# Kernel tuning notes

Measured on AMD Instinct MI355X. Metric: run time of the kernel, lower is better.

## Reference

```python
import jax, jax.numpy as jnp
import numpy as np

N = 262144  # points
C = 256     # backbone_out_channels
K = 20      # semantic_num_classes
BN_EPS = 1e-3
EPS = 1e-8
IGNORE = -1


def setup_inputs() -> dict:
    key = jax.random.key(0)
    ks = jax.random.split(key, 12)
    feat = jax.random.normal(ks[0], (N, C), dtype=jnp.float32)
    coord = jax.random.normal(ks[1], (N, 3), dtype=jnp.float32)
    instance_centroid = jax.random.normal(ks[2], (N, 3), dtype=jnp.float32)
    segment = jax.random.randint(ks[3], (N,), 0, K, dtype=jnp.int32)
    instance = jax.random.randint(ks[4], (N,), 0, 1000, dtype=jnp.int32)
    # bias_head: Linear(C,C) -> BN1d(C) -> ReLU -> Linear(C,3)
    w1 = jax.random.normal(ks[5], (C, C), dtype=jnp.float32) * 0.02
    b1 = jnp.zeros((C,), dtype=jnp.float32)
    gamma = jnp.ones((C,), dtype=jnp.float32)
    beta = jnp.zeros((C,), dtype=jnp.float32)
    w2 = jax.random.normal(ks[6], (C, 3), dtype=jnp.float32) * 0.02
    b2 = jnp.zeros((3,), dtype=jnp.float32)
    # seg_head: Linear(C, K)
    ws = jax.random.normal(ks[7], (C, K), dtype=jnp.float32) * 0.02
    bs = jnp.zeros((K,), dtype=jnp.float32)
    return dict(feat=feat, coord=coord, instance_centroid=instance_centroid,
                segment=segment, instance=instance,
                w1=w1, b1=b1, gamma=gamma, beta=beta, w2=w2, b2=b2, ws=ws, bs=bs)


def reference(feat, coord, instance_centroid, segment, instance,
              w1, b1, gamma, beta, w2, b2, ws, bs):
    # bias head: Linear -> BatchNorm1d (training stats) -> ReLU -> Linear
    h = feat @ w1 + b1                                  # [N, C]
    mu = jnp.mean(h, axis=0)
    var = jnp.mean((h - mu) ** 2, axis=0)               # biased var (torch BN)
    h = (h - mu) * jax.lax.rsqrt(var + BN_EPS) * gamma + beta
    h = jax.nn.relu(h)
    bias_pred = h @ w2 + b2                             # [N, 3]

    logit_pred = feat @ ws + bs                         # [N, K]

    # semantic cross-entropy with ignore_index
    valid = segment != IGNORE
    tgt = jnp.where(valid, segment, 0)
    logp = jax.nn.log_softmax(logit_pred, axis=-1)
    nll = -jnp.take_along_axis(logp, tgt[:, None], axis=1)[:, 0]
    vf = valid.astype(logit_pred.dtype)
    seg_loss = jnp.sum(nll * vf) / (jnp.sum(vf) + EPS)

    # masked bias L1 loss
    mask = (instance != IGNORE).astype(bias_pred.dtype)
    bias_gt = instance_centroid - coord                 # [N, 3]
    bias_dist = jnp.sum(jnp.abs(bias_pred - bias_gt), axis=-1)
    msum = jnp.sum(mask) + EPS
    bias_l1_loss = jnp.sum(bias_dist * mask) / msum

    # masked cosine (direction) loss
    pred_n = bias_pred / (jnp.linalg.norm(bias_pred, axis=1, keepdims=True) + EPS)
    gt_n = bias_gt / (jnp.linalg.norm(bias_gt, axis=1, keepdims=True) + EPS)
    cos = -jnp.sum(pred_n * gt_n, axis=-1)
    bias_cosine_loss = jnp.sum(cos * mask) / msum

    loss = seg_loss + bias_l1_loss + bias_cosine_loss
    return jnp.stack([loss, seg_loss, bias_l1_loss, bias_cosine_loss])
```

## Files before the change

kernel.cpp:

```cpp
#include <hip/hip_runtime.h>
#include <cstdio>
#include <cstdint>

typedef unsigned int u32;
typedef unsigned short u16;
typedef short bf16x8 __attribute__((ext_vector_type(8)));
typedef float f32x4 __attribute__((ext_vector_type(4)));

#define NPTS 262144
#define CDIM 256
#define KCLS 20
#define NBLK 4096
#define NSLOT 256
#define LSLOT 64

#define OFF_WT    ((size_t)134217728)
#define OFF_AGGBN (OFF_WT + (size_t)163840)
#define OFF_AGGNL (OFF_AGGBN + (size_t)524288)
#define OFF_AGGL  (OFF_AGGNL + (size_t)2048)
#define OFF_AB    (OFF_AGGL + (size_t)1024)
#define WS_NEED   (OFF_AB + (size_t)2048)
#define MEMSET_OFF OFF_AGGBN
#define MEMSET_LEN ((size_t)(524288 + 2048 + 1024))

__device__ __forceinline__ u16 bf16rne(float x) {
    u32 u = __float_as_uint(x);
    u32 r = u + 0x7FFFu + ((u >> 16) & 1u);
    return (u16)(r >> 16);
}
__device__ __forceinline__ float bf2f(u16 b) {
    return __uint_as_float(((u32)b) << 16);
}

__global__ void k_prep(const float* __restrict__ w1, const float* __restrict__ wsm,
                       u16* __restrict__ Wt) {
    int k = blockIdx.x;
    int n = threadIdx.x;
    float v = 0.f;
    if (n < 256) v = w1[k * 256 + n];
    else if (n < 256 + KCLS) v = wsm[k * KCLS + (n - 256)];
    Wt[n * 256 + k] = bf16rne(v);
}

__global__ __launch_bounds__(256) void k_gemm(
    const float* __restrict__ feat, const float* __restrict__ b1,
    const float* __restrict__ bs, const int* __restrict__ segment,
    const u16* __restrict__ Wt, u16* __restrict__ h_out,
    float* __restrict__ aggBN, float* __restrict__ aggNLL)
{
    __shared__ uint4 smem4[2112];
    uint4* const As4 = smem4;
    uint4* const Bs4 = smem4 + 256;

    const int t = threadIdx.x;
    const int lane = t & 63;
    const int wv = t >> 6;
    const int q = lane >> 4;
    const int i16 = lane & 15;
    const int row0 = blockIdx.x * 64;
    const int slot = blockIdx.x & (NSLOT - 1);

    const f32x4 fz = {0.f, 0.f, 0.f, 0.f};
    f32x4 acc[4][4];
    f32x4 lacc[2];
#pragma unroll
    for (int r = 0; r < 4; ++r)
#pragma unroll
        for (int c = 0; c < 4; ++c) acc[r][c] = fz;
    lacc[0] = fz; lacc[1] = fz;

    const int sm = t >> 2;
    const int sq = t & 3;
    const float* fsrc = feat + (size_t)(row0 + sm) * 256 + sq * 8;
    const int As_wslot = sq * 64 + (sm ^ (sq << 2));

    float4 f0 = *(const float4*)(fsrc);
    float4 f1 = *(const float4*)(fsrc + 4);

#pragma unroll 1
    for (int kc = 0; kc < 8; ++kc) {
        const int k0 = kc * 32;
        {
            uint4 pk;
            pk.x = (u32)bf16rne(f0.x) | ((u32)bf16rne(f0.y) << 16);
            pk.y = (u32)bf16rne(f0.z) | ((u32)bf16rne(f0.w) << 16);
            pk.z = (u32)bf16rne(f1.x) | ((u32)bf16rne(f1.y) << 16);
            pk.w = (u32)bf16rne(f1.z) | ((u32)bf16rne(f1.w) << 16);
            As4[As_wslot] = pk;
        }
#pragma unroll
        for (int i = 0; i < 5; ++i) {
            const u16* src = Wt + (size_t)(i * 64 + lane) * 256 + k0 + wv * 8;
            u32* dst = (u32*)&Bs4[wv * 320 + i * 64];
            __builtin_amdgcn_global_load_lds(
                (const __attribute__((address_space(1))) u32*)src,
                (__attribute__((address_space(3))) u32*)dst, 16, 0, 0);
        }
        __syncthreads();

        float4 fn0, fn1;
        if (kc < 7) {
            fn0 = *(const float4*)(fsrc + (kc + 1) * 32);
            fn1 = *(const float4*)(fsrc + (kc + 1) * 32 + 4);
        }

        bf16x8 af[4], bfr[4], lbf[2], la;
#pragma unroll
        for (int r = 0; r < 4; ++r)
            af[r] = *(const bf16x8*)&As4[q * 64 + ((r * 16 + i16) ^ (q << 2))];
        la = *(const bf16x8*)&As4[q * 64 + ((wv * 16 + i16) ^ (q << 2))];
#pragma unroll
        for (int c = 0; c < 4; ++c)
            bfr[c] = *(const bf16x8*)&Bs4[q * 320 + wv * 64 + c * 16 + i16];
#pragma unroll
        for (int x = 0; x < 2; ++x)
            lbf[x] = *(const bf16x8*)&Bs4[q * 320 + 256 + x * 16 + i16];

#pragma unroll
        for (int r = 0; r < 4; ++r)
#pragma unroll
            for (int c = 0; c < 4; ++c)
                acc[r][c] = __builtin_amdgcn_mfma_f32_16x16x32_bf16(af[r], bfr[c], acc[r][c], 0, 0, 0);
#pragma unroll
        for (int x = 0; x < 2; ++x)
            lacc[x] = __builtin_amdgcn_mfma_f32_16x16x32_bf16(la, lbf[x], lacc[x], 0, 0, 0);
        __syncthreads();
        f0 = fn0; f1 = fn1;
    }

    float b1v[4];
#pragma unroll
    for (int c = 0; c < 4; ++c) b1v[c] = b1[wv * 64 + c * 16 + i16];
    float bsv0 = bs[i16];
    float bsv1 = (16 + i16 < KCLS) ? bs[16 + i16] : 0.f;

    float nllacc = 0.f, cntacc = 0.f;
#pragma unroll
    for (int j = 0; j < 4; ++j) {
        int rowr = row0 + wv * 16 + q * 4 + j;
        float l0 = lacc[0][j] + bsv0;
        float l1raw = lacc[1][j] + bsv1;
        float l1m = (i16 < 4) ? l1raw : -3.0e38f;
        float mx = fmaxf(l0, l1m);
#pragma unroll
        for (int d = 1; d < 16; d <<= 1) mx = fmaxf(mx, __shfl_xor(mx, d));
        float s = __expf(l0 - mx) + ((i16 < 4) ? __expf(l1raw - mx) : 0.f);
#pragma unroll
        for (int d = 1; d < 16; d <<= 1) s += __shfl_xor(s, d);
        int tg = segment[rowr];
        float v0 = __shfl(l0, (lane & 48) + (tg & 15));
        float v1 = __shfl(l1raw, (lane & 48) + ((tg - 16) & 15));
        float lt = (tg < 16) ? v0 : v1;
        if (i16 == 0 && tg >= 0) {
            nllacc += __logf(s) + mx - lt;
            cntacc += 1.f;
        }
    }
#pragma unroll
    for (int d = 1; d < 64; d <<= 1) {
        nllacc += __shfl_xor(nllacc, d);
        cntacc += __shfl_xor(cntacc, d);
    }
    if (t == 0) { atomicAdd(aggNLL + slot * 2, 0.f); }
    if (lane == 0) {
        atomicAdd(aggNLL + slot * 2 + 0, nllacc);
        atomicAdd(aggNLL + slot * 2 + 1, cntacc);
    }

#pragma unroll
    for (int c = 0; c < 4; ++c) {
        float s1 = 0.f, s2 = 0.f;
#pragma unroll
        for (int r = 0; r < 4; ++r)
#pragma unroll
            for (int j = 0; j < 4; ++j) {
                float v = acc[r][c][j] + b1v[c];
                s1 += v; s2 = fmaf(v, v, s2);
            }
        s1 += __shfl_xor(s1, 16); s1 += __shfl_xor(s1, 32);
        s2 += __shfl_xor(s2, 16); s2 += __shfl_xor(s2, 32);
        if (q == 0) {
            int ch = wv * 64 + c * 16 + i16;
            atomicAdd(aggBN + slot * 512 + ch, s1);
            atomicAdd(aggBN + slot * 512 + 256 + ch, s2);
        }
    }

    u16* Ht = (u16*)smem4;
#pragma unroll
    for (int r = 0; r < 4; ++r)
#pragma unroll
        for (int c = 0; c < 4; ++c)
#pragma unroll
            for (int j = 0; j < 4; ++j) {
                float v = acc[r][c][j] + b1v[c];
                int rw = r * 16 + q * 4 + j;
                int cl = wv * 64 + c * 16 + i16;
                Ht[rw * 264 + cl] = bf16rne(v);
            }
    __syncthreads();
#pragma unroll
    for (int i = 0; i < 8; ++i) {
        int chunk = i * 256 + t;
        int m = chunk >> 5;
        int off = (chunk & 31) * 16;
        uint4 v = *(const uint4*)((const char*)smem4 + m * 528 + off);
        *(uint4*)((char*)h_out + (size_t)(row0 + m) * 512 + off) = v;
    }
}

__global__ void k_reduce(const float* __restrict__ gamma, const float* __restrict__ beta,
                         const float* __restrict__ aggBN,
                         float* __restrict__ Aarr, float* __restrict__ Barr) {
    int c = threadIdx.x;
    float s1 = 0.f, s2 = 0.f;
    for (int s = 0; s < NSLOT; ++s) {
        s1 += aggBN[s * 512 + c];
        s2 += aggBN[s * 512 + 256 + c];
    }
    const float inv = 1.f / (float)NPTS;
    float mu = s1 * inv;
    float var = fmaxf(s2 * inv - mu * mu, 0.f);
    float a = gamma[c] * rsqrtf(var + 1e-3f);
    Aarr[c] = a;
    Barr[c] = beta[c] - mu * a;
}

__global__ __launch_bounds__(256) void k_loss(
    const u16* __restrict__ h, const float* __restrict__ Aarr, const float* __restrict__ Barr,
    const float* __restrict__ w2, const float* __restrict__ b2,
    const float* __restrict__ coord, const float* __restrict__ cent,
    const int* __restrict__ inst, float* __restrict__ aggL)
{
    __shared__ float red[12];
    const int t = threadIdx.x;
    const int lane = t & 63;
    const int wv = t >> 6;
    const int rowbase = blockIdx.x * 128 + wv * 32;
    const int c4 = lane * 4;

    float4 Av = *(const float4*)(Aarr + c4);
    float4 Bv = *(const float4*)(Barr + c4);
    float4 wa = *(const float4*)(w2 + lane * 12);
    float4 wb = *(const float4*)(w2 + lane * 12 + 4);
    float4 wc = *(const float4*)(w2 + lane * 12 + 8);
    float b2x = b2[0], b2y = b2[1], b2z = b2[2];

    float l1a = 0.f, cosa = 0.f, ma = 0.f;
    for (int rr = 0; rr < 32; ++rr) {
        int row = rowbase + rr;
        ushort4 u = *(const ushort4*)(h + (size_t)row * 256 + c4);
        float t0 = fmaxf(fmaf(bf2f(u.x), Av.x, Bv.x), 0.f);
        float t1 = fmaxf(fmaf(bf2f(u.y), Av.y, Bv.y), 0.f);
        float t2 = fmaxf(fmaf(bf2f(u.z), Av.z, Bv.z), 0.f);
        float t3 = fmaxf(fmaf(bf2f(u.w), Av.w, Bv.w), 0.f);
        float p0 = fmaf(t0, wa.x, fmaf(t1, wa.w, fmaf(t2, wb.z, t3 * wc.y)));
        float p1 = fmaf(t0, wa.y, fmaf(t1, wb.x, fmaf(t2, wb.w, t3 * wc.z)));
        float p2 = fmaf(t0, wa.z, fmaf(t1, wb.y, fmaf(t2, wc.x, t3 * wc.w)));
#pragma unroll
        for (int d = 1; d < 64; d <<= 1) {
            p0 += __shfl_xor(p0, d);
            p1 += __shfl_xor(p1, d);
            p2 += __shfl_xor(p2, d);
        }
        if (lane == 0) {
            float bpx = p0 + b2x, bpy = p1 + b2y, bpz = p2 + b2z;
            const float* cp = coord + (size_t)row * 3;
            const float* ip = cent + (size_t)row * 3;
            float gx = ip[0] - cp[0], gy = ip[1] - cp[1], gz = ip[2] - cp[2];
            float mk = (inst[row] != -1) ? 1.f : 0.f;
            float l1 = fabsf(bpx - gx) + fabsf(bpy - gy) + fabsf(bpz - gz);
            float np = sqrtf(fmaf(bpx, bpx, fmaf(bpy, bpy, bpz * bpz)));
            float ng = sqrtf(fmaf(gx, gx, fmaf(gy, gy, gz * gz)));
            float dp = fmaf(bpx, gx, fmaf(bpy, gy, bpz * gz));
            float cosv = -dp / ((np + 1e-8f) * (ng + 1e-8f));
            l1a = fmaf(l1, mk, l1a);
            cosa = fmaf(cosv, mk, cosa);
            ma += mk;
        }
    }
    if (lane == 0) { red[wv] = l1a; red[4 + wv] = cosa; red[8 + wv] = ma; }
    __syncthreads();
    if (t == 0) {
        int slot = blockIdx.x & (LSLOT - 1);
        atomicAdd(aggL + slot * 4 + 0, red[0] + red[1] + red[2] + red[3]);
        atomicAdd(aggL + slot * 4 + 1, red[4] + red[5] + red[6] + red[7]);
        atomicAdd(aggL + slot * 4 + 2, red[8] + red[9] + red[10] + red[11]);
    }
}

__global__ void k_final(const float* __restrict__ aggNLL, const float* __restrict__ aggL,
                        float* __restrict__ out) {
    int lane = threadIdx.x;
    float nll = 0.f, cnt = 0.f;
#pragma unroll
    for (int i = 0; i < 4; ++i) {
        int s = lane + i * 64;
        nll += aggNLL[s * 2 + 0];
        cnt += aggNLL[s * 2 + 1];
    }
    float l1 = aggL[lane * 4 + 0];
    float cs = aggL[lane * 4 + 1];
    float mk = aggL[lane * 4 + 2];
#pragma unroll
    for (int d = 1; d < 64; d <<= 1) {
        nll += __shfl_xor(nll, d);
        cnt += __shfl_xor(cnt, d);
        l1 += __shfl_xor(l1, d);
        cs += __shfl_xor(cs, d);
        mk += __shfl_xor(mk, d);
    }
    if (lane == 0) {
        float seg = nll / (cnt + 1e-8f);
        float l1l = l1 / (mk + 1e-8f);
        float csl = cs / (mk + 1e-8f);
        out[0] = seg + l1l + csl;
        out[1] = seg;
        out[2] = l1l;
        out[3] = csl;
    }
}

extern "C" void kernel_launch(void* const* d_in, const int* in_sizes, int n_in,
                              void* d_out, int out_size, void* d_ws, size_t ws_size,
                              hipStream_t stream) {
    const float* feat   = (const float*)d_in[0];
    const float* coord  = (const float*)d_in[1];
    const float* cent   = (const float*)d_in[2];
    const int* segment  = (const int*)d_in[3];
    const int* inst     = (const int*)d_in[4];
    const float* w1     = (const float*)d_in[5];
    const float* b1     = (const float*)d_in[6];
    const float* gamma  = (const float*)d_in[7];
    const float* beta   = (const float*)d_in[8];
    const float* w2     = (const float*)d_in[9];
    const float* b2     = (const float*)d_in[10];
    const float* wsm    = (const float*)d_in[11];
    const float* bs     = (const float*)d_in[12];
    float* out = (float*)d_out;

    char* wsb = (char*)d_ws;
    u16* h_ws    = (u16*)wsb;
    u16* Wt      = (u16*)(wsb + OFF_WT);
    float* aggBN = (float*)(wsb + OFF_AGGBN);
    float* aggNL = (float*)(wsb + OFF_AGGNL);
    float* aggL  = (float*)(wsb + OFF_AGGL);
    float* Aarr  = (float*)(wsb + OFF_AB);
    float* Barr  = Aarr + 256;

    if (ws_size < WS_NEED)
        fprintf(stderr, "kernel_launch: ws_size=%zu < needed %zu — WILL CORRUPT\n",
                ws_size, (size_t)WS_NEED);

    hipMemsetAsync(wsb + MEMSET_OFF, 0, MEMSET_LEN, stream);
    k_prep<<<256, 320, 0, stream>>>(w1, wsm, Wt);
    k_gemm<<<NBLK, 256, 0, stream>>>(feat, b1, bs, segment, Wt, h_ws, aggBN, aggNL);
    k_reduce<<<1, 256, 0, stream>>>(gamma, beta, aggBN, Aarr, Barr);
    k_loss<<<2048, 256, 0, stream>>>(h_ws, Aarr, Barr, w2, b2, coord, cent, inst, aggL);
    k_final<<<1, 64, 0, stream>>>(aggNL, aggL, out);
}
```

Measured before the change: 550.1 us.

## Double GEMM row tile, parallelize BN reduce, use MFMA for bias head projection

The main GEMM kernel now processes 128 rows per block (two A sub-tiles sharing each B tile load) with an occupancy hint of two blocks per CU, which halves B-tile traffic per row. The BN statistics reduction is spread over 256 blocks with wave shuffles instead of one block looping serially. The loss kernel replaces the per-row 64-lane shuffle reduction with a bf16 MFMA against a zero-padded w2 fragment, processing 16 rows per MFMA. This adds register pressure in the GEMM, and rounding the normalized activations to bf16 before the second linear layer changes precision slightly.

```diff
diff --git a/kernel.cpp b/kernel.cpp
--- a/kernel.cpp
+++ b/kernel.cpp
@@ -10,7 +10,7 @@
 #define NPTS 262144
 #define CDIM 256
 #define KCLS 20
-#define NBLK 4096
+#define NBLK 2048
 #define NSLOT 256
 #define LSLOT 64
 
@@ -42,7 +42,7 @@
     Wt[n * 256 + k] = bf16rne(v);
 }
 
-__global__ __launch_bounds__(256) void k_gemm(
+__global__ __launch_bounds__(256, 2) void k_gemm(
     const float* __restrict__ feat, const float* __restrict__ b1,
     const float* __restrict__ bs, const int* __restrict__ segment,
     const u16* __restrict__ Wt, u16* __restrict__ h_out,
@@ -50,32 +50,36 @@
 {
     __shared__ uint4 smem4[2112];
     uint4* const As4 = smem4;
-    uint4* const Bs4 = smem4 + 256;
+    uint4* const Bs4 = smem4 + 512;
 
     const int t = threadIdx.x;
     const int lane = t & 63;
     const int wv = t >> 6;
     const int q = lane >> 4;
     const int i16 = lane & 15;
-    const int row0 = blockIdx.x * 64;
+    const int row0 = blockIdx.x * 128;
     const int slot = blockIdx.x & (NSLOT - 1);
 
     const f32x4 fz = {0.f, 0.f, 0.f, 0.f};
-    f32x4 acc[4][4];
-    f32x4 lacc[2];
-#pragma unroll
-    for (int r = 0; r < 4; ++r)
+    f32x4 acc[8][4];
+    f32x4 lacc[2][2];
+#pragma unroll
+    for (int r = 0; r < 8; ++r)
 #pragma unroll
         for (int c = 0; c < 4; ++c) acc[r][c] = fz;
-    lacc[0] = fz; lacc[1] = fz;
+    lacc[0][0] = fz; lacc[0][1] = fz; lacc[1][0] = fz; lacc[1][1] = fz;
 
     const int sm = t >> 2;
     const int sq = t & 3;
-    const float* fsrc = feat + (size_t)(row0 + sm) * 256 + sq * 8;
-    const int As_wslot = sq * 64 + (sm ^ (sq << 2));
-
-    float4 f0 = *(const float4*)(fsrc);
-    float4 f1 = *(const float4*)(fsrc + 4);
+    const float* fsrcA = feat + (size_t)(row0 + sm) * 256 + sq * 8;
+    const float* fsrcB = feat + (size_t)(row0 + 64 + sm) * 256 + sq * 8;
+    const int As_wslotA = sq * 128 + (sm ^ (sq << 2));
+    const int As_wslotB = sq * 128 + ((sm + 64) ^ (sq << 2));
+
+    float4 f0 = *(const float4*)(fsrcA);
+    float4 f1 = *(const float4*)(fsrcA + 4);
+    float4 g0 = *(const float4*)(fsrcB);
+    float4 g1 = *(const float4*)(fsrcB + 4);
 
 #pragma unroll 1
     for (int kc = 0; kc < 8; ++kc) {
@@ -86,7 +90,12 @@
             pk.y = (u32)bf16rne(f0.z) | ((u32)bf16rne(f0.w) << 16);
             pk.z = (u32)bf16rne(f1.x) | ((u32)bf16rne(f1.y) << 16);
             pk.w = (u32)bf16rne(f1.z) | ((u32)bf16rne(f1.w) << 16);
-            As4[As_wslot] = pk;
+            As4[As_wslotA] = pk;
+            pk.x = (u32)bf16rne(g0.x) | ((u32)bf16rne(g0.y) << 16);
+            pk.y = (u32)bf16rne(g0.z) | ((u32)bf16rne(g0.w) << 16);
+            pk.z = (u32)bf16rne(g1.x) | ((u32)bf16rne(g1.y) << 16);
+            pk.w = (u32)bf16rne(g1.z) | ((u32)bf16rne(g1.w) << 16);
+            As4[As_wslotB] = pk;
         }
 #pragma unroll
         for (int i = 0; i < 5; ++i) {
@@ -98,17 +107,15 @@
         }
         __syncthreads();
 
-        float4 fn0, fn1;
+        float4 fn0, fn1, gn0, gn1;
         if (kc < 7) {
-            fn0 = *(const float4*)(fsrc + (kc + 1) * 32);
-            fn1 = *(const float4*)(fsrc + (kc + 1) * 32 + 4);
-        }
-
-        bf16x8 af[4], bfr[4], lbf[2], la;
-#pragma unroll
-        for (int r = 0; r < 4; ++r)
-            af[r] = *(const bf16x8*)&As4[q * 64 + ((r * 16 + i16) ^ (q << 2))];
-        la = *(const bf16x8*)&As4[q * 64 + ((wv * 16 + i16) ^ (q << 2))];
+            fn0 = *(const float4*)(fsrcA + (kc + 1) * 32);
+            fn1 = *(const float4*)(fsrcA + (kc + 1) * 32 + 4);
+            gn0 = *(const float4*)(fsrcB + (kc + 1) * 32);
+            gn1 = *(const float4*)(fsrcB + (kc + 1) * 32 + 4);
+        }
+
+        bf16x8 bfr[4], lbf[2];
 #pragma unroll
         for (int c = 0; c < 4; ++c)
             bfr[c] = *(const bf16x8*)&Bs4[q * 320 + wv * 64 + c * 16 + i16];
@@ -117,15 +124,21 @@
             lbf[x] = *(const bf16x8*)&Bs4[q * 320 + 256 + x * 16 + i16];
 
 #pragma unroll
-        for (int r = 0; r < 4; ++r)
+        for (int r = 0; r < 8; ++r) {
+            bf16x8 af = *(const bf16x8*)&As4[q * 128 + ((r * 16 + i16) ^ (q << 2))];
 #pragma unroll
             for (int c = 0; c < 4; ++c)
-                acc[r][c] = __builtin_amdgcn_mfma_f32_16x16x32_bf16(af[r], bfr[c], acc[r][c], 0, 0, 0);
-#pragma unroll
-        for (int x = 0; x < 2; ++x)
-            lacc[x] = __builtin_amdgcn_mfma_f32_16x16x32_bf16(la, lbf[x], lacc[x], 0, 0, 0);
+                acc[r][c] = __builtin_amdgcn_mfma_f32_16x16x32_bf16(af, bfr[c], acc[r][c], 0, 0, 0);
+        }
+#pragma unroll
+        for (int lt = 0; lt < 2; ++lt) {
+            bf16x8 la = *(const bf16x8*)&As4[q * 128 + ((wv * 32 + lt * 16 + i16) ^ (q << 2))];
+#pragma unroll
+            for (int x = 0; x < 2; ++x)
+                lacc[lt][x] = __builtin_amdgcn_mfma_f32_16x16x32_bf16(la, lbf[x], lacc[lt][x], 0, 0, 0);
+        }
         __syncthreads();
-        f0 = fn0; f1 = fn1;
+        f0 = fn0; f1 = fn1; g0 = gn0; g1 = gn1;
     }
 
     float b1v[4];
@@ -136,10 +149,12 @@
 
     float nllacc = 0.f, cntacc = 0.f;
 #pragma unroll
+    for (int lt = 0; lt < 2; ++lt)
+#pragma unroll
     for (int j = 0; j < 4; ++j) {
-        int rowr = row0 + wv * 16 + q * 4 + j;
-        float l0 = lacc[0][j] + bsv0;
-        float l1raw = lacc[1][j] + bsv1;
+        int rowr = row0 + wv * 32 + lt * 16 + q * 4 + j;
+        float l0 = lacc[lt][0][j] + bsv0;
+        float l1raw = lacc[lt][1][j] + bsv1;
         float l1m = (i16 < 4) ? l1raw : -3.0e38f;
         float mx = fmaxf(l0, l1m);
 #pragma unroll
@@ -150,9 +165,9 @@
         int tg = segment[rowr];
         float v0 = __shfl(l0, (lane & 48) + (tg & 15));
         float v1 = __shfl(l1raw, (lane & 48) + ((tg - 16) & 15));
-        float lt = (tg < 16) ? v0 : v1;
+        float lt_ = (tg < 16) ? v0 : v1;
         if (i16 == 0 && tg >= 0) {
-            nllacc += __logf(s) + mx - lt;
+            nllacc += __logf(s) + mx - lt_;
             cntacc += 1.f;
         }
     }
@@ -161,7 +176,6 @@
         nllacc += __shfl_xor(nllacc, d);
         cntacc += __shfl_xor(cntacc, d);
     }
-    if (t == 0) { atomicAdd(aggNLL + slot * 2, 0.f); }
     if (lane == 0) {
         atomicAdd(aggNLL + slot * 2 + 0, nllacc);
         atomicAdd(aggNLL + slot * 2 + 1, cntacc);
@@ -171,7 +185,7 @@
     for (int c = 0; c < 4; ++c) {
         float s1 = 0.f, s2 = 0.f;
 #pragma unroll
-        for (int r = 0; r < 4; ++r)
+        for (int r = 0; r < 8; ++r)
 #pragma unroll
             for (int j = 0; j < 4; ++j) {
                 float v = acc[r][c][j] + b1v[c];
@@ -187,43 +201,57 @@
     }
 
     u16* Ht = (u16*)smem4;
-#pragma unroll
-    for (int r = 0; r < 4; ++r)
-#pragma unroll
-        for (int c = 0; c < 4; ++c)
-#pragma unroll
-            for (int j = 0; j < 4; ++j) {
-                float v = acc[r][c][j] + b1v[c];
-                int rw = r * 16 + q * 4 + j;
-                int cl = wv * 64 + c * 16 + i16;
-                Ht[rw * 264 + cl] = bf16rne(v);
-            }
-    __syncthreads();
-#pragma unroll
-    for (int i = 0; i < 8; ++i) {
-        int chunk = i * 256 + t;
-        int m = chunk >> 5;
-        int off = (chunk & 31) * 16;
-        uint4 v = *(const uint4*)((const char*)smem4 + m * 528 + off);
-        *(uint4*)((char*)h_out + (size_t)(row0 + m) * 512 + off) = v;
+#pragma unroll 1
+    for (int p = 0; p < 2; ++p) {
+#pragma unroll
+        for (int r = p * 4; r < p * 4 + 4; ++r)
+#pragma unroll
+            for (int c = 0; c < 4; ++c)
+#pragma unroll
+                for (int j = 0; j < 4; ++j) {
+                    float v = acc[r][c][j] + b1v[c];
+                    int rw = (r - p * 4) * 16 + q * 4 + j;
+                    int cl = wv * 64 + c * 16 + i16;
+                    Ht[rw * 264 + cl] = bf16rne(v);
+                }
+        __syncthreads();
+#pragma unroll
+        for (int i = 0; i < 8; ++i) {
+            int chunk = i * 256 + t;
+            int m = chunk >> 5;
+            int off = (chunk & 31) * 16;
+            uint4 v = *(const uint4*)((const char*)smem4 + m * 528 + off);
+            *(uint4*)((char*)h_out + (size_t)(row0 + p * 64 + m) * 512 + off) = v;
+        }
+        __syncthreads();
     }
 }
 
 __global__ void k_reduce(const float* __restrict__ gamma, const float* __restrict__ beta,
                          const float* __restrict__ aggBN,
                          float* __restrict__ Aarr, float* __restrict__ Barr) {
-    int c = threadIdx.x;
+    int c = blockIdx.x;
+    int l = threadIdx.x;
     float s1 = 0.f, s2 = 0.f;
-    for (int s = 0; s < NSLOT; ++s) {
+#pragma unroll
+    for (int i = 0; i < 4; ++i) {
+        int s = l + i * 64;
         s1 += aggBN[s * 512 + c];
         s2 += aggBN[s * 512 + 256 + c];
     }
-    const float inv = 1.f / (float)NPTS;
-    float mu = s1 * inv;
-    float var = fmaxf(s2 * inv - mu * mu, 0.f);
-    float a = gamma[c] * rsqrtf(var + 1e-3f);
-    Aarr[c] = a;
-    Barr[c] = beta[c] - mu * a;
+#pragma unroll
+    for (int d = 1; d < 64; d <<= 1) {
+        s1 += __shfl_xor(s1, d);
+        s2 += __shfl_xor(s2, d);
+    }
+    if (l == 0) {
+        const float inv = 1.f / (float)NPTS;
+        float mu = s1 * inv;
+        float var = fmaxf(s2 * inv - mu * mu, 0.f);
+        float a = gamma[c] * rsqrtf(var + 1e-3f);
+        Aarr[c] = a;
+        Barr[c] = beta[c] - mu * a;
+    }
 }
 
 __global__ __launch_bounds__(256) void k_loss(
@@ -232,39 +260,68 @@
     const float* __restrict__ coord, const float* __restrict__ cent,
     const int* __restrict__ inst, float* __restrict__ aggL)
 {
+    __shared__ float w2s[768];
+    __shared__ float As_l[256], Bs_l[256];
+    __shared__ float bp[4][16][4];
     __shared__ float red[12];
+
     const int t = threadIdx.x;
     const int lane = t & 63;
     const int wv = t >> 6;
-    const int rowbase = blockIdx.x * 128 + wv * 32;
-    const int c4 = lane * 4;
-
-    float4 Av = *(const float4*)(Aarr + c4);
-    float4 Bv = *(const float4*)(Barr + c4);
-    float4 wa = *(const float4*)(w2 + lane * 12);
-    float4 wb = *(const float4*)(w2 + lane * 12 + 4);
-    float4 wc = *(const float4*)(w2 + lane * 12 + 8);
+    const int q = lane >> 4;
+    const int i16 = lane & 15;
+
+    if (t < 256) { As_l[t] = Aarr[t]; Bs_l[t] = Barr[t]; }
+    for (int i = t; i < 768; i += 256) w2s[i] = w2[i];
+    __syncthreads();
+
+    bf16x8 wfr[8];
+#pragma unroll
+    for (int kc = 0; kc < 8; ++kc) {
+        bf16x8 f;
+#pragma unroll
+        for (int j = 0; j < 8; ++j) {
+            int k = kc * 32 + q * 8 + j;
+            float v = (i16 < 3) ? w2s[k * 3 + i16] : 0.f;
+            ((u16*)&f)[j] = bf16rne(v);
+        }
+        wfr[kc] = f;
+    }
     float b2x = b2[0], b2y = b2[1], b2z = b2[2];
 
+    const f32x4 fz = {0.f, 0.f, 0.f, 0.f};
     float l1a = 0.f, cosa = 0.f, ma = 0.f;
-    for (int rr = 0; rr < 32; ++rr) {
-        int row = rowbase + rr;
-        ushort4 u = *(const ushort4*)(h + (size_t)row * 256 + c4);
-        float t0 = fmaxf(fmaf(bf2f(u.x), Av.x, Bv.x), 0.f);
-        float t1 = fmaxf(fmaf(bf2f(u.y), Av.y, Bv.y), 0.f);
-        float t2 = fmaxf(fmaf(bf2f(u.z), Av.z, Bv.z), 0.f);
-        float t3 = fmaxf(fmaf(bf2f(u.w), Av.w, Bv.w), 0.f);
-        float p0 = fmaf(t0, wa.x, fmaf(t1, wa.w, fmaf(t2, wb.z, t3 * wc.y)));
-        float p1 = fmaf(t0, wa.y, fmaf(t1, wb.x, fmaf(t2, wb.w, t3 * wc.z)));
-        float p2 = fmaf(t0, wa.z, fmaf(t1, wb.y, fmaf(t2, wc.x, t3 * wc.w)));
-#pragma unroll
-        for (int d = 1; d < 64; d <<= 1) {
-            p0 += __shfl_xor(p0, d);
-            p1 += __shfl_xor(p1, d);
-            p2 += __shfl_xor(p2, d);
-        }
-        if (lane == 0) {
-            float bpx = p0 + b2x, bpy = p1 + b2y, bpz = p2 + b2z;
+
+    const int wavebase = blockIdx.x * 256 + wv * 64;
+#pragma unroll 1
+    for (int g = 0; g < 4; ++g) {
+        const int rb = wavebase + g * 16;
+        f32x4 c = fz;
+#pragma unroll
+        for (int kc = 0; kc < 8; ++kc) {
+            bf16x8 hf = *(const bf16x8*)(h + (size_t)(rb + i16) * 256 + kc * 32 + q * 8);
+            float4 a0 = *(const float4*)(As_l + kc * 32 + q * 8);
+            float4 a1 = *(const float4*)(As_l + kc * 32 + q * 8 + 4);
+            float4 b0 = *(const float4*)(Bs_l + kc * 32 + q * 8);
+            float4 b1 = *(const float4*)(Bs_l + kc * 32 + q * 8 + 4);
+            float av[8] = {a0.x, a0.y, a0.z, a0.w, a1.x, a1.y, a1.z, a1.w};
+            float bv[8] = {b0.x, b0.y, b0.z, b0.w, b1.x, b1.y, b1.z, b1.w};
+            bf16x8 hn;
+#pragma unroll
+            for (int j = 0; j < 8; ++j) {
+                float x = fmaxf(fmaf(bf2f(((const u16*)&hf)[j]), av[j], bv[j]), 0.f);
+                ((u16*)&hn)[j] = bf16rne(x);
+            }
+            c = __builtin_amdgcn_mfma_f32_16x16x32_bf16(hn, wfr[kc], c, 0, 0, 0);
+        }
+        if (i16 < 3) {
+#pragma unroll
+            for (int j = 0; j < 4; ++j) bp[wv][q * 4 + j][i16] = c[j];
+        }
+        if (lane < 16) {
+            int row = rb + lane;
+            float4 P = *(const float4*)bp[wv][lane];
+            float bpx = P.x + b2x, bpy = P.y + b2y, bpz = P.z + b2z;
             const float* cp = coord + (size_t)row * 3;
             const float* ip = cent + (size_t)row * 3;
             float gx = ip[0] - cp[0], gy = ip[1] - cp[1], gz = ip[2] - cp[2];
@@ -278,6 +335,12 @@
             cosa = fmaf(cosv, mk, cosa);
             ma += mk;
         }
+    }
+#pragma unroll
+    for (int d = 1; d < 64; d <<= 1) {
+        l1a += __shfl_xor(l1a, d);
+        cosa += __shfl_xor(cosa, d);
+        ma += __shfl_xor(ma, d);
     }
     if (lane == 0) { red[wv] = l1a; red[4 + wv] = cosa; red[8 + wv] = ma; }
     __syncthreads();
@@ -355,7 +418,7 @@
     hipMemsetAsync(wsb + MEMSET_OFF, 0, MEMSET_LEN, stream);
     k_prep<<<256, 320, 0, stream>>>(w1, wsm, Wt);
     k_gemm<<<NBLK, 256, 0, stream>>>(feat, b1, bs, segment, Wt, h_ws, aggBN, aggNL);
-    k_reduce<<<1, 256, 0, stream>>>(gamma, beta, aggBN, Aarr, Barr);
-    k_loss<<<2048, 256, 0, stream>>>(h_ws, Aarr, Barr, w2, b2, coord, cent, inst, aggL);
+    k_reduce<<<256, 64, 0, stream>>>(gamma, beta, aggBN, Aarr, Barr);
+    k_loss<<<1024, 256, 0, stream>>>(h_ws, Aarr, Barr, w2, b2, coord, cent, inst, aggL);
     k_final<<<1, 64, 0, stream>>>(aggNL, aggL, out);
 }
```

Result: slower. 823.5 us (+49.7%).
